# Kernel optimization log

Hardware: AMD Instinct MI355X
Metric: run time of the kernel (lower is better)

The kernel has to match this reference:

```python
import jax, jax.numpy as jnp
from jax import lax
import numpy as np

B, H, W = 16, 512, 512
OPENING_R, EROSION_R, DILATION_R = 5, 2, 1
MIN_SIZE, AREA_THRESHOLD = 2000, 300
INF = np.int32(2 ** 30)


def _disk(r):
    # skimage.morphology.disk: x^2 + y^2 <= r^2 on a (2r+1)^2 grid
    y, x = np.mgrid[-r:r + 1, -r:r + 1]
    return jnp.asarray((x * x + y * y <= r * r).astype(np.float32))


D_OPEN, D_ERODE, D_DILATE = _disk(OPENING_R), _disk(EROSION_R), _disk(DILATION_R)


def _conv2(x, k):
    return lax.conv_general_dilated(x[None, None], k[None, None], (1, 1), 'VALID')[0, 0]


def _erode(fg, se):
    # skimage binary_erosion uses border_value=True (image border does not erode)
    r = se.shape[0] // 2
    x = jnp.pad(fg.astype(jnp.float32), r, constant_values=1.0)
    return _conv2(x, se) >= se.sum() - 0.5


def _dilate(fg, se):
    # skimage binary_dilation uses border_value=False
    r = se.shape[0] // 2
    x = jnp.pad(fg.astype(jnp.float32), r, constant_values=0.0)
    return _conv2(x, se) > 0.5


def _seg_cummin(v, reset, axis, reverse):
    # segmented cumulative-min: scan resets wherever `reset` is True (background)
    def comb(a, b):
        av, af = a
        bv, bf = b
        return jnp.where(bf, bv, jnp.minimum(av, bv)), af | bf

    vv, _ = lax.associative_scan(comb, (v, reset), axis=axis, reverse=reverse)
    return vv


def _label(fg):
    # 4-connectivity connected-component labeling via min-label propagation.
    # Each fg pixel starts with its raveled index; alternating row/col segmented
    # cummin sweeps run under while_loop until a fixed point (root id per comp).
    h, w = fg.shape
    idx = jnp.arange(h * w, dtype=jnp.int32).reshape(h, w)
    lab0 = jnp.where(fg, idx, INF)
    bg = ~fg

    def sweep(l):
        for axis in (1, 0):
            for rev in (False, True):
                l = jnp.where(fg, _seg_cummin(l, bg, axis, rev), INF)
        return l

    def body(c):
        l, _ = c
        nl = sweep(l)
        return nl, jnp.array_equal(nl, l)

    lab, _ = lax.while_loop(lambda c: ~c[1], body, (lab0, jnp.array(False)))
    seg = jnp.where(fg, lab, 0).ravel()
    sizes = jax.ops.segment_sum(fg.astype(jnp.int32).ravel(), seg, num_segments=h * w)
    ncomp = jnp.sum(sizes > 0)
    return lab, sizes, ncomp


def _remove_small_objects(fg, min_size, guard):
    lab, sizes, ncomp = _label(fg)
    px = sizes[jnp.where(fg, lab, 0)]  # component size at every fg pixel
    kept = fg & (px >= min_size)
    # original only removes small objects when label(...).max() > 1
    return jnp.where(ncomp > 1, kept, fg) if guard else kept


def _pipeline(mask):
    fg = mask > 0
    fg = _remove_small_objects(fg, MIN_SIZE, True)
    # remove_small_holes == ~remove_small_objects(~fg, area_threshold + 1)
    fg = ~_remove_small_objects(~fg, AREA_THRESHOLD + 1, False)
    fg = _erode(fg, D_ERODE)
    fg = _dilate(_erode(fg, D_OPEN), D_OPEN)  # binary_opening
    fg = _remove_small_objects(fg, MIN_SIZE, True)
    fg = _dilate(fg, D_DILATE)
    return fg.astype(jnp.float32)  # original casts to int; float32 kept for vjp parity


def setup_inputs() -> dict:
    key = jax.random.key(0)
    # blobby binary masks: threshold bilinearly-upsampled low-res noise so that
    # realistic large connected components (> min_size px) exist
    low = jax.random.uniform(key, (B, H // 16, W // 16), dtype=jnp.float32)
    blob = jax.image.resize(low, (B, H, W), method='bilinear')
    return {'inputs': (blob > 0.5).astype(jnp.float32)}


def reference(inputs):
    return jax.vmap(_pipeline)(inputs)
```

## Files before the change

kernel.cpp:

```cpp
#include <hip/hip_runtime.h>
#include <stdint.h>

#define BATCH 16
#define H 512
#define W 512
#define HW (H * W)
#define NTOT (BATCH * HW)
#define NWORDS (NTOT / 64)

#define TPB 256
#define NBLK ((NTOT + TPB - 1) / TPB)
#define NBLKW ((NWORDS + TPB - 1) / TPB)

#define SROWS 16
#define SWORDS 128
#define SPIX 8192
#define NSTRIPS (NWORDS / SWORDS)

__device__ __forceinline__ int find_root_c(int* L, int x) {
    int r = x, p = L[r];
    while (p != r) { r = p; p = L[r]; }
    if (L[x] != r) atomicMin(&L[x], r);
    return r;
}

__device__ void merge_uf(int* L, int a, int b) {
    while (true) {
        a = find_root_c(L, a);
        b = find_root_c(L, b);
        if (a == b) return;
        int lo = a < b ? a : b;
        int hi = a < b ? b : a;
        int old = atomicMin(&L[hi], lo);
        if (old == hi) return;
        a = lo; b = old;
    }
}

__device__ __forceinline__ int find_root_lds(int* P, int x) {
    int r = x, p = P[r];
    while (p != r) { r = p; p = P[r]; }
    return r;
}

__device__ void merge_lds(int* P, int a, int b) {
    while (true) {
        a = find_root_lds(P, a);
        b = find_root_lds(P, b);
        if (a == b) return;
        int lo = a < b ? a : b;
        int hi = a < b ? b : a;
        int old = atomicMin(&P[hi], lo);
        if (old == hi) return;
        a = lo; b = old;
    }
}

__device__ __forceinline__ int start_of(uint64_t m, int i, int cv, int base) {
    uint64_t below = i ? ((~m) & ((1ull << i) - 1)) : 0ull;
    if (below == 0) return (cv >= 0) ? cv : base;
    int hz = 63 - __builtin_clzll(below);
    return base + hz + 1;
}

__global__ void k_thresh_pack(const float* __restrict__ in, uint64_t* __restrict__ bits) {
    int p = blockIdx.x * blockDim.x + threadIdx.x;
    bool a = (p < NTOT) && (in[p] > 0.0f);
    uint64_t b = __ballot(a);
    if ((threadIdx.x & 63) == 0 && p < NTOT) bits[p >> 6] = b;
}

__global__ void k_strip_ccl(const uint64_t* __restrict__ bits, int inv,
                            int* __restrict__ carry, int* __restrict__ L,
                            int* __restrict__ sizes, int* __restrict__ ncomp) {
    __shared__ uint64_t sw[SWORDS];
    __shared__ int scarry[SWORDS];
    __shared__ int par[SPIX];
    int blk = blockIdx.x;
    int t = threadIdx.x;
    int gw = blk * SWORDS + t;
    uint64_t inv64 = inv ? ~0ull : 0ull;
    uint64_t m = bits[gw] ^ inv64;
    sw[t] = m;
    __syncthreads();

    if (t < SROWS) {
        int cv = -1;
        for (int i = 0; i < 8; ++i) {
            int lw = t * 8 + i;
            scarry[lw] = cv;
            uint64_t w = sw[lw];
            if (w >> 63) {
                uint64_t z = ~w;
                if (z == 0) { if (cv < 0) cv = lw << 6; }
                else { int hz = 63 - __builtin_clzll(z); cv = (lw << 6) + hz + 1; }
            } else cv = -1;
        }
    }
    __syncthreads();

    int cv = scarry[t];
    carry[gw] = (cv >= 0) ? (blk * SPIX + cv) : -1;
    int lbase = t << 6;
    uint64_t starts = m & ~((m << 1) | ((cv >= 0) ? 1ull : 0ull));
    uint64_t ss = starts;
    while (ss) {
        int s = __builtin_ctzll(ss);
        par[lbase + s] = lbase + s;
        ss &= ss - 1;
    }
    __syncthreads();

    if (t >= 8 && m) {
        uint64_t up = sw[t - 8];
        uint64_t cand = m & up;
        if (cand) {
            uint64_t curprev = (t & 7) ? sw[t - 1] : 0ull;
            uint64_t upprev  = (t & 7) ? sw[t - 9] : 0ull;
            uint64_t curl = (m << 1) | (curprev >> 63);
            uint64_t upl  = (up << 1) | (upprev >> 63);
            cand &= ~(curl & upl);
            int cvu = scarry[t - 8];
            while (cand) {
                int i = __builtin_ctzll(cand);
                int sP = start_of(m, i, cv, lbase);
                int sQ = start_of(up, i, cvu, lbase - 512);
                merge_lds(par, sP, sQ);
                cand &= cand - 1;
            }
        }
    }
    __syncthreads();

    int gpix = blk * SPIX;
    ss = starts;
    while (ss) {
        int s = __builtin_ctzll(ss);
        int ls = lbase + s;
        int r = find_root_lds(par, ls);
        L[gpix + ls] = gpix + r;
        if (r == ls) sizes[gpix + ls] = 0;
        ss &= ss - 1;
    }
    if (t == 0 && (blk & 31) == 0) ncomp[blk >> 5] = 0;
}

__global__ void k_merge_bound(const uint64_t* __restrict__ bits, int inv,
                              const int* __restrict__ carry, int* __restrict__ L) {
    int gw = blockIdx.x * blockDim.x + threadIdx.x;
    if (gw >= NWORDS) return;
    int wrow = gw & 7;
    int y = (gw >> 3) & (H - 1);
    if (y == 0 || (y & (SROWS - 1))) return;
    uint64_t inv64 = inv ? ~0ull : 0ull;
    uint64_t cur = bits[gw] ^ inv64;
    uint64_t up  = bits[gw - 8] ^ inv64;
    uint64_t cand = cur & up;
    if (!cand) return;
    uint64_t curprev = wrow ? (bits[gw - 1] ^ inv64) : 0ull;
    uint64_t upprev  = wrow ? (bits[gw - 9] ^ inv64) : 0ull;
    uint64_t curl = (cur << 1) | (curprev >> 63);
    uint64_t upl  = (up << 1)  | (upprev >> 63);
    cand &= ~(curl & upl);
    if (!cand) return;
    int cvc = carry[gw], cvu = carry[gw - 8];
    int base = gw << 6;
    while (cand) {
        int i = __builtin_ctzll(cand);
        int sP = start_of(cur, i, cvc, base);
        int sQ = start_of(up, i, cvu, base - W);
        merge_uf(L, sP, sQ);
        cand &= cand - 1;
    }
}

__global__ void k_flatten_count(const uint64_t* __restrict__ bits, int inv,
                                const int* __restrict__ carry, int* __restrict__ L,
                                int* __restrict__ sizes, int* __restrict__ ncomp) {
    __shared__ int hk[128];
    __shared__ int hv[128];
    for (int i = threadIdx.x; i < 128; i += TPB) { hk[i] = -1; hv[i] = 0; }
    __syncthreads();

    int gw = blockIdx.x * blockDim.x + threadIdx.x;
    if (gw < NWORDS) {
        uint64_t inv64 = inv ? ~0ull : 0ull;
        uint64_t m = bits[gw] ^ inv64;
        if (m) {
            int cv = carry[gw];
            int base = gw << 6;
            while (m) {
                int s = __builtin_ctzll(m);
                uint64_t rest = m >> s;
                uint64_t nr = ~rest;
                int len = nr ? __builtin_ctzll(nr) : (64 - s);
                uint64_t piece = ((len >= 64) ? ~0ull : ((1ull << len) - 1)) << s;
                bool initial = !(s == 0 && cv >= 0);
                int start = initial ? (base + s) : cv;
                int r = find_root_c(L, start);
                if (initial && r == start) atomicAdd(&ncomp[gw >> 12], 1);
                int cnt = __popcll(piece);
                uint32_t h = ((uint32_t)r * 2654435761u) >> 25;
                bool done = false;
                for (int t = 0; t < 16; ++t) {
                    int slot = (h + t) & 127;
                    int k = hk[slot];
                    if (k == -1) k = atomicCAS(&hk[slot], -1, r);
                    if (k == -1 || k == r) { atomicAdd(&hv[slot], cnt); done = true; break; }
                }
                if (!done) atomicAdd(&sizes[r], cnt);
                m &= ~piece;
            }
        }
    }
    __syncthreads();
    for (int i = threadIdx.x; i < 128; i += TPB)
        if (hk[i] != -1) atomicAdd(&sizes[hk[i]], hv[i]);
}

__global__ void k_keep_guard(const uint64_t* __restrict__ bits,
                             const int* __restrict__ carry, const int* __restrict__ L,
                             const int* __restrict__ sizes, const int* __restrict__ ncomp,
                             int minsz, uint64_t* __restrict__ out) {
    int gw = blockIdx.x * blockDim.x + threadIdx.x;
    if (gw >= NWORDS) return;
    uint64_t m = bits[gw];
    uint64_t res = m;
    if (m && ncomp[gw >> 12] > 1) {
        int cv = carry[gw];
        int base = gw << 6;
        while (m) {
            int s = __builtin_ctzll(m);
            uint64_t rest = m >> s;
            uint64_t nr = ~rest;
            int len = nr ? __builtin_ctzll(nr) : (64 - s);
            uint64_t piece = ((len >= 64) ? ~0ull : ((1ull << len) - 1)) << s;
            int start = (s == 0 && cv >= 0) ? cv : (base + s);
            int r = L[start];
            if (sizes[r] < minsz) res &= ~piece;
            m &= ~piece;
        }
    }
    out[gw] = res;
}

__global__ void k_fill_holes(const uint64_t* __restrict__ bits,
                             const int* __restrict__ carry, const int* __restrict__ L,
                             const int* __restrict__ sizes, int minsz,
                             uint64_t* __restrict__ out) {
    int gw = blockIdx.x * blockDim.x + threadIdx.x;
    if (gw >= NWORDS) return;
    uint64_t fg = bits[gw];
    uint64_t bg = ~fg;
    uint64_t res = fg;
    int cv = carry[gw];
    int base = gw << 6;
    while (bg) {
        int s = __builtin_ctzll(bg);
        uint64_t rest = bg >> s;
        uint64_t nr = ~rest;
        int len = nr ? __builtin_ctzll(nr) : (64 - s);
        uint64_t piece = ((len >= 64) ? ~0ull : ((1ull << len) - 1)) << s;
        int start = (s == 0 && cv >= 0) ? cv : (base + s);
        int r = L[start];
        if (sizes[r] < minsz) res |= piece;
        bg &= ~piece;
    }
    out[gw] = res;
}

template <int R, bool ERODE>
__global__ void k_morph_bits(const uint64_t* __restrict__ in, uint64_t* __restrict__ out) {
    int gw = blockIdx.x * blockDim.x + threadIdx.x;
    if (gw >= NWORDS) return;
    int w = gw & 7;
    int y = (gw >> 3) & (H - 1);
    int b = gw >> 12;
    const uint64_t* img = in + (size_t)b * H * 8;
    const uint64_t BORDER = ERODE ? ~0ull : 0ull;
    uint64_t res = ERODE ? ~0ull : 0ull;
#pragma unroll
    for (int dy = -R; dy <= R; ++dy) {
        int yy = y + dy;
        if (yy < 0 || yy >= H) continue;
        int v = R * R - dy * dy;
        int kx = 0;
        while ((kx + 1) * (kx + 1) <= v) ++kx;
        uint64_t cur = img[yy * 8 + w];
        uint64_t prv = (w > 0) ? img[yy * 8 + w - 1] : BORDER;
        uint64_t nxt = (w < 7) ? img[yy * 8 + w + 1] : BORDER;
        uint64_t acc = cur;
#pragma unroll
        for (int dx = 1; dx <= kx; ++dx) {
            uint64_t right = (cur >> dx) | (nxt << (64 - dx));
            uint64_t left  = (cur << dx) | (prv >> (64 - dx));
            if (ERODE) acc &= right & left;
            else       acc |= right | left;
        }
        if (ERODE) res &= acc;
        else       res |= acc;
    }
    out[gw] = res;
}

__global__ void k_to_float_dilate(const uint64_t* __restrict__ bits,
                                  float* __restrict__ out) {
    int p = blockIdx.x * blockDim.x + threadIdx.x;
    if (p >= NTOT) return;
    int gw = p >> 6;
    int i = p & 63;
    int w = gw & 7;
    int y = (gw >> 3) & (H - 1);
    uint64_t cur = bits[gw];
    uint64_t up  = (y > 0)     ? bits[gw - 8] : 0ull;
    uint64_t dn  = (y < H - 1) ? bits[gw + 8] : 0ull;
    uint64_t prv = (w > 0)     ? bits[gw - 1] : 0ull;
    uint64_t nxt = (w < 7)     ? bits[gw + 1] : 0ull;
    uint64_t d = cur | up | dn | (cur << 1) | (prv >> 63) | (cur >> 1) | (nxt << 63);
    out[p] = ((d >> i) & 1ull) ? 1.0f : 0.0f;
}

static void run_ccl(const uint64_t* mask, int inv, int* carry, int* labels,
                    int* sizes, int* ncomp, hipStream_t stream) {
    k_strip_ccl<<<NSTRIPS, SWORDS, 0, stream>>>(mask, inv, carry, labels, sizes, ncomp);
    k_merge_bound<<<NBLKW, TPB, 0, stream>>>(mask, inv, carry, labels);
    k_flatten_count<<<NBLKW, TPB, 0, stream>>>(mask, inv, carry, labels, sizes, ncomp);
}

extern "C" void kernel_launch(void* const* d_in, const int* in_sizes, int n_in,
                              void* d_out, int out_size, void* d_ws, size_t ws_size,
                              hipStream_t stream) {
    const float* in = (const float*)d_in[0];
    float* out = (float*)d_out;

    uint8_t* ws = (uint8_t*)d_ws;
    int* labels = (int*)ws;
    int* sizes  = (int*)(ws + (size_t)NTOT * 4);
    uint64_t* bitsA = (uint64_t*)(ws + (size_t)NTOT * 8);
    uint64_t* bitsB = bitsA + NWORDS;
    int* carry = (int*)(bitsB + NWORDS);
    int* ncomp = carry + NWORDS;

    k_thresh_pack<<<NBLK, TPB, 0, stream>>>(in, bitsA);

    run_ccl(bitsA, 0, carry, labels, sizes, ncomp, stream);
    k_keep_guard<<<NBLKW, TPB, 0, stream>>>(bitsA, carry, labels, sizes, ncomp, 2000, bitsB);

    run_ccl(bitsB, 1, carry, labels, sizes, ncomp, stream);
    k_fill_holes<<<NBLKW, TPB, 0, stream>>>(bitsB, carry, labels, sizes, 301, bitsA);

    k_morph_bits<2, true><<<NBLKW, TPB, 0, stream>>>(bitsA, bitsB);
    k_morph_bits<5, true><<<NBLKW, TPB, 0, stream>>>(bitsB, bitsA);
    k_morph_bits<5, false><<<NBLKW, TPB, 0, stream>>>(bitsA, bitsB);

    run_ccl(bitsB, 0, carry, labels, sizes, ncomp, stream);
    k_keep_guard<<<NBLKW, TPB, 0, stream>>>(bitsB, carry, labels, sizes, ncomp, 2000, bitsA);

    k_to_float_dilate<<<NBLK, TPB, 0, stream>>>(bitsA, out);
}
```

Baseline: 210.7 us.

## Fuse threshold into strip CCL, fill+morphology chain in LDS, keep into final dilate

Fuses the threshold/bit-pack into the first strip CCL kernel. It merges hole filling with the erode/erode/dilate chain into one tiled kernel that keeps a haloed 88-row tile in LDS. It also folds the last keep-guard into the float-output dilation, where lanes cooperatively compute neighbour words and share them with shuffles. k_merge_bound is relaunched with one block per image that touches only strip-boundary rows. Together these cut kernel launches and global round-trips, at the cost of redundant halo work in the fused morph kernel and in the final keep step.

```diff
diff --git a/kernel.cpp b/kernel.cpp
--- a/kernel.cpp
+++ b/kernel.cpp
@@ -63,24 +63,83 @@
     return base + hz + 1;
 }
 
-__global__ void k_thresh_pack(const float* __restrict__ in, uint64_t* __restrict__ bits) {
-    int p = blockIdx.x * blockDim.x + threadIdx.x;
-    bool a = (p < NTOT) && (in[p] > 0.0f);
-    uint64_t b = __ballot(a);
-    if ((threadIdx.x & 63) == 0 && p < NTOT) bits[p >> 6] = b;
-}
-
-__global__ void k_strip_ccl(const uint64_t* __restrict__ bits, int inv,
-                            int* __restrict__ carry, int* __restrict__ L,
-                            int* __restrict__ sizes, int* __restrict__ ncomp) {
-    __shared__ uint64_t sw[SWORDS];
-    __shared__ int scarry[SWORDS];
-    __shared__ int par[SPIX];
-    int blk = blockIdx.x;
-    int t = threadIdx.x;
-    int gw = blk * SWORDS + t;
-    uint64_t inv64 = inv ? ~0ull : 0ull;
-    uint64_t m = bits[gw] ^ inv64;
+__device__ uint64_t keep_word(const uint64_t* __restrict__ bits,
+                              const int* __restrict__ carry, const int* __restrict__ L,
+                              const int* __restrict__ sizes, const int* __restrict__ ncomp,
+                              int minsz, int gw) {
+    uint64_t m = bits[gw];
+    uint64_t res = m;
+    if (m && ncomp[gw >> 12] > 1) {
+        int cv = carry[gw];
+        int base = gw << 6;
+        while (m) {
+            int s = __builtin_ctzll(m);
+            uint64_t rest = m >> s;
+            uint64_t nr = ~rest;
+            int len = nr ? __builtin_ctzll(nr) : (64 - s);
+            uint64_t piece = ((len >= 64) ? ~0ull : ((1ull << len) - 1)) << s;
+            int start = (s == 0 && cv >= 0) ? cv : (base + s);
+            if (sizes[L[start]] < minsz) res &= ~piece;
+            m &= ~piece;
+        }
+    }
+    return res;
+}
+
+__device__ uint64_t fill_word(const uint64_t* __restrict__ bits,
+                              const int* __restrict__ carry, const int* __restrict__ L,
+                              const int* __restrict__ sizes, int minsz, int gw) {
+    uint64_t fg = bits[gw];
+    uint64_t bg = ~fg;
+    uint64_t res = fg;
+    int cv = carry[gw];
+    int base = gw << 6;
+    while (bg) {
+        int s = __builtin_ctzll(bg);
+        uint64_t rest = bg >> s;
+        uint64_t nr = ~rest;
+        int len = nr ? __builtin_ctzll(nr) : (64 - s);
+        uint64_t piece = ((len >= 64) ? ~0ull : ((1ull << len) - 1)) << s;
+        int start = (s == 0 && cv >= 0) ? cv : (base + s);
+        if (sizes[L[start]] < minsz) res |= piece;
+        bg &= ~piece;
+    }
+    return res;
+}
+
+template <int R, bool ERODE>
+__device__ uint64_t morph_word_lds(const uint64_t* buf, int lrow, int w, int gyTop) {
+    const uint64_t BORDER = ERODE ? ~0ull : 0ull;
+    uint64_t res = ERODE ? ~0ull : 0ull;
+#pragma unroll
+    for (int dy = -R; dy <= R; ++dy) {
+        int lr = lrow + dy;
+        int gy = gyTop + lr;
+        if (gy < 0 || gy >= H) continue;
+        int v = R * R - dy * dy;
+        int kx = 0;
+        while ((kx + 1) * (kx + 1) <= v) ++kx;
+        uint64_t cur = buf[lr * 8 + w];
+        uint64_t prv = (w > 0) ? buf[lr * 8 + w - 1] : BORDER;
+        uint64_t nxt = (w < 7) ? buf[lr * 8 + w + 1] : BORDER;
+        uint64_t acc = cur;
+#pragma unroll
+        for (int dx = 1; dx <= kx; ++dx) {
+            uint64_t right = (cur >> dx) | (nxt << (64 - dx));
+            uint64_t left  = (cur << dx) | (prv >> (64 - dx));
+            if (ERODE) acc &= right & left;
+            else       acc |= right | left;
+        }
+        if (ERODE) res &= acc;
+        else       res |= acc;
+    }
+    return res;
+}
+
+__device__ void strip_ccl_body(uint64_t m, uint64_t* sw, int* scarry, int* par,
+                               int blk, int t,
+                               int* __restrict__ carry, int* __restrict__ L,
+                               int* __restrict__ sizes, int* __restrict__ ncomp) {
     sw[t] = m;
     __syncthreads();
 
@@ -100,7 +159,7 @@
     __syncthreads();
 
     int cv = scarry[t];
-    carry[gw] = (cv >= 0) ? (blk * SPIX + cv) : -1;
+    carry[blk * SWORDS + t] = (cv >= 0) ? (blk * SPIX + cv) : -1;
     int lbase = t << 6;
     uint64_t starts = m & ~((m << 1) | ((cv >= 0) ? 1ull : 0ull));
     uint64_t ss = starts;
@@ -145,20 +204,56 @@
     if (t == 0 && (blk & 31) == 0) ncomp[blk >> 5] = 0;
 }
 
+
+__global__ void k_thresh_ccl(const float* __restrict__ in, uint64_t* __restrict__ bits,
+                             int* __restrict__ carry, int* __restrict__ L,
+                             int* __restrict__ sizes, int* __restrict__ ncomp) {
+    __shared__ uint64_t sw[SWORDS];
+    __shared__ int scarry[SWORDS];
+    __shared__ int par[SPIX];
+    int blk = blockIdx.x;
+    int t = threadIdx.x;
+    int wave = t >> 6, lane = t & 63;
+    size_t stripPix = (size_t)blk * SPIX;
+    for (int k = 0; k < 64; ++k) {
+        bool a = in[stripPix + wave * 4096 + k * 64 + lane] > 0.0f;
+        uint64_t b = __ballot(a);
+        if (lane == 0) sw[wave * 64 + k] = b;
+    }
+    __syncthreads();
+    uint64_t m = sw[t];
+    bits[blk * SWORDS + t] = m;
+    strip_ccl_body(m, sw, scarry, par, blk, t, carry, L, sizes, ncomp);
+}
+
+__global__ void k_strip_ccl(const uint64_t* __restrict__ bits, int inv,
+                            int* __restrict__ carry, int* __restrict__ L,
+                            int* __restrict__ sizes, int* __restrict__ ncomp) {
+    __shared__ uint64_t sw[SWORDS];
+    __shared__ int scarry[SWORDS];
+    __shared__ int par[SPIX];
+    int blk = blockIdx.x;
+    int t = threadIdx.x;
+    uint64_t inv64 = inv ? ~0ull : 0ull;
+    uint64_t m = bits[blk * SWORDS + t] ^ inv64;
+    strip_ccl_body(m, sw, scarry, par, blk, t, carry, L, sizes, ncomp);
+}
+
 __global__ void k_merge_bound(const uint64_t* __restrict__ bits, int inv,
                               const int* __restrict__ carry, int* __restrict__ L) {
-    int gw = blockIdx.x * blockDim.x + threadIdx.x;
-    if (gw >= NWORDS) return;
-    int wrow = gw & 7;
-    int y = (gw >> 3) & (H - 1);
-    if (y == 0 || (y & (SROWS - 1))) return;
+    int tid = threadIdx.x;
+    if (tid >= 248) return;
+    int img = blockIdx.x;
+    int y = ((tid >> 3) + 1) * SROWS;
+    int w = tid & 7;
+    int gw = img * 4096 + y * 8 + w;
     uint64_t inv64 = inv ? ~0ull : 0ull;
     uint64_t cur = bits[gw] ^ inv64;
     uint64_t up  = bits[gw - 8] ^ inv64;
     uint64_t cand = cur & up;
     if (!cand) return;
-    uint64_t curprev = wrow ? (bits[gw - 1] ^ inv64) : 0ull;
-    uint64_t upprev  = wrow ? (bits[gw - 9] ^ inv64) : 0ull;
+    uint64_t curprev = w ? (bits[gw - 1] ^ inv64) : 0ull;
+    uint64_t upprev  = w ? (bits[gw - 9] ^ inv64) : 0ull;
     uint64_t curl = (cur << 1) | (curprev >> 63);
     uint64_t upl  = (up << 1)  | (upprev >> 63);
     cand &= ~(curl & upl);
@@ -202,8 +297,8 @@
                 int cnt = __popcll(piece);
                 uint32_t h = ((uint32_t)r * 2654435761u) >> 25;
                 bool done = false;
-                for (int t = 0; t < 16; ++t) {
-                    int slot = (h + t) & 127;
+                for (int tt = 0; tt < 16; ++tt) {
+                    int slot = (h + tt) & 127;
                     int k = hk[slot];
                     if (k == -1) k = atomicCAS(&hk[slot], -1, r);
                     if (k == -1 || k == r) { atomicAdd(&hv[slot], cnt); done = true; break; }
@@ -224,107 +319,79 @@
                              int minsz, uint64_t* __restrict__ out) {
     int gw = blockIdx.x * blockDim.x + threadIdx.x;
     if (gw >= NWORDS) return;
-    uint64_t m = bits[gw];
-    uint64_t res = m;
-    if (m && ncomp[gw >> 12] > 1) {
-        int cv = carry[gw];
-        int base = gw << 6;
-        while (m) {
-            int s = __builtin_ctzll(m);
-            uint64_t rest = m >> s;
-            uint64_t nr = ~rest;
-            int len = nr ? __builtin_ctzll(nr) : (64 - s);
-            uint64_t piece = ((len >= 64) ? ~0ull : ((1ull << len) - 1)) << s;
-            int start = (s == 0 && cv >= 0) ? cv : (base + s);
-            int r = L[start];
-            if (sizes[r] < minsz) res &= ~piece;
-            m &= ~piece;
-        }
-    }
-    out[gw] = res;
-}
-
-__global__ void k_fill_holes(const uint64_t* __restrict__ bits,
+    out[gw] = keep_word(bits, carry, L, sizes, ncomp, minsz, gw);
+}
+
+__global__ void k_fill_morph(const uint64_t* __restrict__ bits,
                              const int* __restrict__ carry, const int* __restrict__ L,
-                             const int* __restrict__ sizes, int minsz,
+                             const int* __restrict__ sizes,
                              uint64_t* __restrict__ out) {
-    int gw = blockIdx.x * blockDim.x + threadIdx.x;
-    if (gw >= NWORDS) return;
-    uint64_t fg = bits[gw];
-    uint64_t bg = ~fg;
-    uint64_t res = fg;
-    int cv = carry[gw];
-    int base = gw << 6;
-    while (bg) {
-        int s = __builtin_ctzll(bg);
-        uint64_t rest = bg >> s;
-        uint64_t nr = ~rest;
-        int len = nr ? __builtin_ctzll(nr) : (64 - s);
-        uint64_t piece = ((len >= 64) ? ~0ull : ((1ull << len) - 1)) << s;
-        int start = (s == 0 && cv >= 0) ? cv : (base + s);
-        int r = L[start];
-        if (sizes[r] < minsz) res |= piece;
-        bg &= ~piece;
-    }
-    out[gw] = res;
-}
-
-template <int R, bool ERODE>
-__global__ void k_morph_bits(const uint64_t* __restrict__ in, uint64_t* __restrict__ out) {
-    int gw = blockIdx.x * blockDim.x + threadIdx.x;
-    if (gw >= NWORDS) return;
-    int w = gw & 7;
-    int y = (gw >> 3) & (H - 1);
-    int b = gw >> 12;
-    const uint64_t* img = in + (size_t)b * H * 8;
-    const uint64_t BORDER = ERODE ? ~0ull : 0ull;
-    uint64_t res = ERODE ? ~0ull : 0ull;
-#pragma unroll
-    for (int dy = -R; dy <= R; ++dy) {
-        int yy = y + dy;
-        if (yy < 0 || yy >= H) continue;
-        int v = R * R - dy * dy;
-        int kx = 0;
-        while ((kx + 1) * (kx + 1) <= v) ++kx;
-        uint64_t cur = img[yy * 8 + w];
-        uint64_t prv = (w > 0) ? img[yy * 8 + w - 1] : BORDER;
-        uint64_t nxt = (w < 7) ? img[yy * 8 + w + 1] : BORDER;
-        uint64_t acc = cur;
-#pragma unroll
-        for (int dx = 1; dx <= kx; ++dx) {
-            uint64_t right = (cur >> dx) | (nxt << (64 - dx));
-            uint64_t left  = (cur << dx) | (prv >> (64 - dx));
-            if (ERODE) acc &= right & left;
-            else       acc |= right | left;
-        }
-        if (ERODE) res &= acc;
-        else       res |= acc;
-    }
-    out[gw] = res;
-}
-
-__global__ void k_to_float_dilate(const uint64_t* __restrict__ bits,
-                                  float* __restrict__ out) {
+    __shared__ uint64_t bufA[88 * 8];
+    __shared__ uint64_t bufB[88 * 8];
+    int img = blockIdx.x >> 3;
+    int s   = blockIdx.x & 7;
+    int y0 = s * 64;
+    int gyTop = y0 - 12;
+    int t = threadIdx.x;
+
+    for (int lw = t; lw < 88 * 8; lw += TPB) {
+        int gy = gyTop + (lw >> 3);
+        int w = lw & 7;
+        uint64_t v = 0;
+        if (gy >= 0 && gy < H)
+            v = fill_word(bits, carry, L, sizes, 301, img * 4096 + gy * 8 + w);
+        bufA[lw] = v;
+    }
+    __syncthreads();
+
+    for (int lw = t; lw < 88 * 8; lw += TPB) {
+        int lr = lw >> 3;
+        if (lr < 2 || lr > 85) continue;
+        bufB[lw] = morph_word_lds<2, true>(bufA, lr, lw & 7, gyTop);
+    }
+    __syncthreads();
+
+    for (int lw = t; lw < 88 * 8; lw += TPB) {
+        int lr = lw >> 3;
+        if (lr < 7 || lr > 80) continue;
+        bufA[lw] = morph_word_lds<5, true>(bufB, lr, lw & 7, gyTop);
+    }
+    __syncthreads();
+
+    for (int lw = t; lw < 88 * 8; lw += TPB) {
+        int lr = lw >> 3;
+        if (lr < 12 || lr > 75) continue;
+        uint64_t v = morph_word_lds<5, false>(bufA, lr, lw & 7, gyTop);
+        int gy = gyTop + lr;
+        out[img * 4096 + gy * 8 + (lw & 7)] = v;
+    }
+}
+
+__global__ void k_keep_dilate_float(const uint64_t* __restrict__ bits,
+                                    const int* __restrict__ carry, const int* __restrict__ L,
+                                    const int* __restrict__ sizes, const int* __restrict__ ncomp,
+                                    float* __restrict__ out) {
     int p = blockIdx.x * blockDim.x + threadIdx.x;
     if (p >= NTOT) return;
     int gw = p >> 6;
-    int i = p & 63;
+    int lane = threadIdx.x & 63;
     int w = gw & 7;
     int y = (gw >> 3) & (H - 1);
-    uint64_t cur = bits[gw];
-    uint64_t up  = (y > 0)     ? bits[gw - 8] : 0ull;
-    uint64_t dn  = (y < H - 1) ? bits[gw + 8] : 0ull;
-    uint64_t prv = (w > 0)     ? bits[gw - 1] : 0ull;
-    uint64_t nxt = (w < 7)     ? bits[gw + 1] : 0ull;
+    int target = -1;
+    if      (lane == 0) target = gw;
+    else if (lane == 1) target = (y > 0)     ? gw - 8 : -1;
+    else if (lane == 2) target = (y < H - 1) ? gw + 8 : -1;
+    else if (lane == 3) target = (w > 0)     ? gw - 1 : -1;
+    else if (lane == 4) target = (w < 7)     ? gw + 1 : -1;
+    uint64_t tv = (target >= 0)
+        ? keep_word(bits, carry, L, sizes, ncomp, 2000, target) : 0ull;
+    uint64_t cur = __shfl(tv, 0);
+    uint64_t up  = __shfl(tv, 1);
+    uint64_t dn  = __shfl(tv, 2);
+    uint64_t prv = __shfl(tv, 3);
+    uint64_t nxt = __shfl(tv, 4);
     uint64_t d = cur | up | dn | (cur << 1) | (prv >> 63) | (cur >> 1) | (nxt << 63);
-    out[p] = ((d >> i) & 1ull) ? 1.0f : 0.0f;
-}
-
-static void run_ccl(const uint64_t* mask, int inv, int* carry, int* labels,
-                    int* sizes, int* ncomp, hipStream_t stream) {
-    k_strip_ccl<<<NSTRIPS, SWORDS, 0, stream>>>(mask, inv, carry, labels, sizes, ncomp);
-    k_merge_bound<<<NBLKW, TPB, 0, stream>>>(mask, inv, carry, labels);
-    k_flatten_count<<<NBLKW, TPB, 0, stream>>>(mask, inv, carry, labels, sizes, ncomp);
+    out[p] = ((d >> lane) & 1ull) ? 1.0f : 0.0f;
 }
 
 extern "C" void kernel_launch(void* const* d_in, const int* in_sizes, int n_in,
@@ -341,20 +408,20 @@
     int* carry = (int*)(bitsB + NWORDS);
     int* ncomp = carry + NWORDS;
 
-    k_thresh_pack<<<NBLK, TPB, 0, stream>>>(in, bitsA);
-
-    run_ccl(bitsA, 0, carry, labels, sizes, ncomp, stream);
+    k_thresh_ccl<<<NSTRIPS, SWORDS, 0, stream>>>(in, bitsA, carry, labels, sizes, ncomp);
+    k_merge_bound<<<BATCH, 256, 0, stream>>>(bitsA, 0, carry, labels);
+    k_flatten_count<<<NBLKW, TPB, 0, stream>>>(bitsA, 0, carry, labels, sizes, ncomp);
     k_keep_guard<<<NBLKW, TPB, 0, stream>>>(bitsA, carry, labels, sizes, ncomp, 2000, bitsB);
 
-    run_ccl(bitsB, 1, carry, labels, sizes, ncomp, stream);
-    k_fill_holes<<<NBLKW, TPB, 0, stream>>>(bitsB, carry, labels, sizes, 301, bitsA);
-
-    k_morph_bits<2, true><<<NBLKW, TPB, 0, stream>>>(bitsA, bitsB);
-    k_morph_bits<5, true><<<NBLKW, TPB, 0, stream>>>(bitsB, bitsA);
-    k_morph_bits<5, false><<<NBLKW, TPB, 0, stream>>>(bitsA, bitsB);
-
-    run_ccl(bitsB, 0, carry, labels, sizes, ncomp, stream);
-    k_keep_guard<<<NBLKW, TPB, 0, stream>>>(bitsB, carry, labels, sizes, ncomp, 2000, bitsA);
-
-    k_to_float_dilate<<<NBLK, TPB, 0, stream>>>(bitsA, out);
-}
+    k_strip_ccl<<<NSTRIPS, SWORDS, 0, stream>>>(bitsB, 1, carry, labels, sizes, ncomp);
+    k_merge_bound<<<BATCH, 256, 0, stream>>>(bitsB, 1, carry, labels);
+    k_flatten_count<<<NBLKW, TPB, 0, stream>>>(bitsB, 1, carry, labels, sizes, ncomp);
+
+    k_fill_morph<<<BATCH * 8, TPB, 0, stream>>>(bitsB, carry, labels, sizes, bitsA);
+
+    k_strip_ccl<<<NSTRIPS, SWORDS, 0, stream>>>(bitsA, 0, carry, labels, sizes, ncomp);
+    k_merge_bound<<<BATCH, 256, 0, stream>>>(bitsA, 0, carry, labels);
+    k_flatten_count<<<NBLKW, TPB, 0, stream>>>(bitsA, 0, carry, labels, sizes, ncomp);
+
+    k_keep_dilate_float<<<NBLK, TPB, 0, stream>>>(bitsA, carry, labels, sizes, ncomp, out);
+}
```

Measured after the change: 231.9 us. 1.1x slower.
